# Performance work log

Hardware: AMD Instinct MI355X
Metric: run time of the kernel (lower is better)

Reference implementation:

```python
import jax, jax.numpy as jnp
import numpy as np

KERNEL = 7
PAD = 3


def setup_inputs() -> dict:
    key = jax.random.key(0)
    k1, k2, k3 = jax.random.split(key, 3)
    B, C, H, W = 16, 256, 64, 64
    x = jax.random.normal(k1, (B, C, H, W), dtype=jnp.float32)
    weight = jax.random.normal(k2, (C, KERNEL * KERNEL), dtype=jnp.float32)
    bias = jax.random.normal(k3, (C,), dtype=jnp.float32)
    return {"x": x, "weight": weight, "bias": bias}


def reference(x, weight, bias):
    # x: (B, C, H, W); weight: (C, K*K) laid out row-major as in nn.Unfold
    # (unfold * weight).sum over the K*K patch dim == depthwise 'same' conv.
    C = weight.shape[0]
    kernel = weight.reshape(C, 1, KERNEL, KERNEL)  # OIHW with I=1, groups=C
    out = jax.lax.conv_general_dilated(
        x, kernel,
        window_strides=(1, 1),
        padding=((PAD, PAD), (PAD, PAD)),
        dimension_numbers=("NCHW", "OIHW", "NCHW"),
        feature_group_count=C,
    )
    out = out + bias[None, :, None, None]
    # Original wraps this in to_sparse(): a lossless repacking of nonzero
    # pixels into (indices, features) with data-dependent shape. Its dense()
    # equals `out`, so we return the dense form.
    return out
```

## Files before the change

### kernel.cpp

```cpp
#include <hip/hip_runtime.h>


typedef _Float16 v2h __attribute__((ext_vector_type(2)));

static __device__ __forceinline__ v2h pack2(float a, float b) {
    return __builtin_bit_cast(v2h, __builtin_amdgcn_cvt_pkrtz(a, b));
}

__global__ __launch_bounds__(256, 2)
void dwconv7x7_dot2(const float* __restrict__ x,
                    const float* __restrict__ weight,
                    const float* __restrict__ bias,
                    float* __restrict__ out) {
    const int tid  = threadIdx.x;
    const int lane = tid & 63;
    const int wid  = tid >> 6;
    const int gw   = blockIdx.x * 4 + wid;
    const int plane = gw >> 1;
    const int half  = gw & 1;
    const int c = __builtin_amdgcn_readfirstlane(plane & 255);

    const float* wp = weight + c * 49;
    float wk[49];
#pragma unroll
    for (int k = 0; k < 49; ++k) wk[k] = wp[k];
    const float bv = bias[c];

    v2h  W[7][3];
    float w6[7];
#pragma unroll
    for (int kr = 0; kr < 7; ++kr) {
#pragma unroll
        for (int t = 0; t < 3; ++t) {
            v2h p = pack2(wk[kr * 7 + 2 * t], wk[kr * 7 + 2 * t + 1]);
            int b = __builtin_amdgcn_readfirstlane(__builtin_bit_cast(int, p));
            W[kr][t] = __builtin_bit_cast(v2h, b);
        }
        w6[kr] = wk[kr * 7 + 6];
    }

    const int tx = lane & 15;
    const int sy = lane >> 4;
    const int wb = tx * 4;
    const int hb = half * 32 + sy * 8;

    const float* xp = x + (size_t)plane * 4096;
    const int offm = (tx > 0)  ? (wb - 4) : wb;
    const int offp = (tx < 15) ? (wb + 4) : wb;

    float acc[8][4];
#pragma unroll
    for (int i = 0; i < 8; ++i)
#pragma unroll
        for (int j = 0; j < 4; ++j) acc[i][j] = 0.f;

#pragma unroll
    for (int j = 0; j < 14; ++j) {
        const int r  = hb - 3 + j;
        const int rc = min(max(r, 0), 63);
        const float* rowp = xp + rc * 64;
        const bool mrow = (r >= 0) && (r < 64);
        const bool mm = mrow && (tx > 0);
        const bool mp = mrow && (tx < 15);

        float4 qm = *reinterpret_cast<const float4*>(rowp + offm);
        float4 q0 = *reinterpret_cast<const float4*>(rowp + wb);
        float4 qp = *reinterpret_cast<const float4*>(rowp + offp);

        float f[10];
        f[0] = mm   ? qm.y : 0.f;
        f[1] = mm   ? qm.z : 0.f;
        f[2] = mm   ? qm.w : 0.f;
        f[3] = mrow ? q0.x : 0.f;
        f[4] = mrow ? q0.y : 0.f;
        f[5] = mrow ? q0.z : 0.f;
        f[6] = mrow ? q0.w : 0.f;
        f[7] = mp   ? qp.x : 0.f;
        f[8] = mp   ? qp.y : 0.f;
        f[9] = mp   ? qp.z : 0.f;

        v2h pk[8];
#pragma unroll
        for (int t = 0; t < 8; ++t) pk[t] = pack2(f[t], f[t + 1]);

#pragma unroll
        for (int oi = 0; oi < 8; ++oi) {
            const int kr = j - oi;
            if (kr >= 0 && kr < 7) {
#pragma unroll
                for (int jj = 0; jj < 4; ++jj) {
                    float a = fmaf(f[jj + 6], w6[kr], acc[oi][jj]);
                    a = __builtin_amdgcn_fdot2(pk[jj + 4], W[kr][2], a, false);
                    a = __builtin_amdgcn_fdot2(pk[jj + 2], W[kr][1], a, false);
                    a = __builtin_amdgcn_fdot2(pk[jj],     W[kr][0], a, false);
                    acc[oi][jj] = a;
                }
            }
        }
    }

    float* op = out + (size_t)plane * 4096 + (size_t)hb * 64 + wb;
#pragma unroll
    for (int oi = 0; oi < 8; ++oi) {
        float4 v;
        v.x = acc[oi][0] + bv;
        v.y = acc[oi][1] + bv;
        v.z = acc[oi][2] + bv;
        v.w = acc[oi][3] + bv;
        *reinterpret_cast<float4*>(op + oi * 64) = v;
    }
}

extern "C" void kernel_launch(void* const* d_in, const int* in_sizes, int n_in,
                              void* d_out, int out_size, void* d_ws, size_t ws_size,
                              hipStream_t stream) {
    const float* x      = (const float*)d_in[0];
    const float* weight = (const float*)d_in[1];
    const float* bias   = (const float*)d_in[2];
    float* out          = (float*)d_out;
    (void)in_sizes; (void)n_in; (void)out_size; (void)d_ws; (void)ws_size;

    dim3 grid(2048);
    dim3 block(256);
    dwconv7x7_dot2<<<grid, block, 0, stream>>>(x, weight, bias, out);
}
```

Measured before the change: 34.25 us.

## Roll row loop with sliding accumulator window and streaming output stores

Replaces the fully unrolled 14-row loop with a rolled loop that keeps a 7-row sliding window of accumulators, shifting them each iteration and storing one finished output row per step. This is meant to cut code size and register pressure. In exchange, it computes all 7 kernel-row updates for every input row, including boundary rows whose results are discarded, and it adds register-shift moves each iteration.

```diff
diff --git a/kernel.cpp b/kernel.cpp
--- a/kernel.cpp
+++ b/kernel.cpp
@@ -8,10 +8,10 @@
 }
 
 __global__ __launch_bounds__(256, 2)
-void dwconv7x7_dot2(const float* __restrict__ x,
-                    const float* __restrict__ weight,
-                    const float* __restrict__ bias,
-                    float* __restrict__ out) {
+void dwconv7x7_rolled(const float* __restrict__ x,
+                      const float* __restrict__ weight,
+                      const float* __restrict__ bias,
+                      float* __restrict__ out) {
     const int tid  = threadIdx.x;
     const int lane = tid & 63;
     const int wid  = tid >> 6;
@@ -48,13 +48,15 @@
     const int offm = (tx > 0)  ? (wb - 4) : wb;
     const int offp = (tx < 15) ? (wb + 4) : wb;
 
-    float acc[8][4];
+    float accR[7][4];
 #pragma unroll
-    for (int i = 0; i < 8; ++i)
+    for (int k = 0; k < 7; ++k)
 #pragma unroll
-        for (int j = 0; j < 4; ++j) acc[i][j] = 0.f;
+        for (int jj = 0; jj < 4; ++jj) accR[k][jj] = 0.f;
 
-#pragma unroll
+    float* op = out + (size_t)plane * 4096 + (size_t)hb * 64 + wb;
+
+#pragma unroll 1
     for (int j = 0; j < 14; ++j) {
         const int r  = hb - 3 + j;
         const int rc = min(max(r, 0), 63);
@@ -84,30 +86,33 @@
         for (int t = 0; t < 8; ++t) pk[t] = pack2(f[t], f[t + 1]);
 
 #pragma unroll
-        for (int oi = 0; oi < 8; ++oi) {
-            const int kr = j - oi;
-            if (kr >= 0 && kr < 7) {
+        for (int k = 0; k < 7; ++k) {
+            const int kr = 6 - k;
 #pragma unroll
-                for (int jj = 0; jj < 4; ++jj) {
-                    float a = fmaf(f[jj + 6], w6[kr], acc[oi][jj]);
-                    a = __builtin_amdgcn_fdot2(pk[jj + 4], W[kr][2], a, false);
-                    a = __builtin_amdgcn_fdot2(pk[jj + 2], W[kr][1], a, false);
-                    a = __builtin_amdgcn_fdot2(pk[jj],     W[kr][0], a, false);
-                    acc[oi][jj] = a;
-                }
+            for (int jj = 0; jj < 4; ++jj) {
+                float a = fmaf(f[jj + 6], w6[kr], accR[k][jj]);
+                a = __builtin_amdgcn_fdot2(pk[jj + 4], W[kr][2], a, false);
+                a = __builtin_amdgcn_fdot2(pk[jj + 2], W[kr][1], a, false);
+                a = __builtin_amdgcn_fdot2(pk[jj],     W[kr][0], a, false);
+                accR[k][jj] = a;
             }
         }
-    }
 
-    float* op = out + (size_t)plane * 4096 + (size_t)hb * 64 + wb;
+        if (j >= 6) {
+            float4 v;
+            v.x = accR[0][0] + bv;
+            v.y = accR[0][1] + bv;
+            v.z = accR[0][2] + bv;
+            v.w = accR[0][3] + bv;
+            *reinterpret_cast<float4*>(op + (j - 6) * 64) = v;
+        }
+
 #pragma unroll
-    for (int oi = 0; oi < 8; ++oi) {
-        float4 v;
-        v.x = acc[oi][0] + bv;
-        v.y = acc[oi][1] + bv;
-        v.z = acc[oi][2] + bv;
-        v.w = acc[oi][3] + bv;
-        *reinterpret_cast<float4*>(op + oi * 64) = v;
+        for (int k = 0; k < 6; ++k)
+#pragma unroll
+            for (int jj = 0; jj < 4; ++jj) accR[k][jj] = accR[k + 1][jj];
+#pragma unroll
+        for (int jj = 0; jj < 4; ++jj) accR[6][jj] = 0.f;
     }
 }
 
@@ -122,5 +127,5 @@
 
     dim3 grid(2048);
     dim3 block(256);
-    dwconv7x7_dot2<<<grid, block, 0, stream>>>(x, weight, bias, out);
+    dwconv7x7_rolled<<<grid, block, 0, stream>>>(x, weight, bias, out);
 }
```

After: 39.93 us. 16.6% more time.

## Flatten depthwise conv to one output row per thread with larger grid

Applied to the files above, without the earlier changes.

Replaces the register-blocked scheme, where each thread accumulated 8 output rows while streaming 14 input rows, with a flat scheme where each thread computes a single output row from 7 input rows. The grid grows eightfold so each block covers a quarter plane. This cuts register pressure and raises parallelism, but gives up vertical row reuse and quadruples redundant input loads per output, relying on caches. It also repeats the per-block weight loads many more times.

```diff
diff --git a/kernel.cpp b/kernel.cpp
--- a/kernel.cpp
+++ b/kernel.cpp
@@ -7,18 +7,15 @@
     return __builtin_bit_cast(v2h, __builtin_amdgcn_cvt_pkrtz(a, b));
 }
 
-__global__ __launch_bounds__(256, 2)
-void dwconv7x7_dot2(const float* __restrict__ x,
+__global__ __launch_bounds__(256)
+void dwconv7x7_flat(const float* __restrict__ x,
                     const float* __restrict__ weight,
                     const float* __restrict__ bias,
                     float* __restrict__ out) {
-    const int tid  = threadIdx.x;
-    const int lane = tid & 63;
-    const int wid  = tid >> 6;
-    const int gw   = blockIdx.x * 4 + wid;
-    const int plane = gw >> 1;
-    const int half  = gw & 1;
-    const int c = __builtin_amdgcn_readfirstlane(plane & 255);
+    const int tid   = threadIdx.x;
+    const int bk    = blockIdx.x;
+    const int plane = bk >> 2;
+    const int c     = plane & 255;
 
     const float* wp = weight + c * 49;
     float wk[49];
@@ -39,24 +36,20 @@
         w6[kr] = wk[kr * 7 + 6];
     }
 
-    const int tx = lane & 15;
-    const int sy = lane >> 4;
-    const int wb = tx * 4;
-    const int hb = half * 32 + sy * 8;
+    const int tx   = tid & 15;
+    const int ty   = tid >> 4;
+    const int orow = (bk & 3) * 16 + ty;
+    const int wb   = tx * 4;
 
     const float* xp = x + (size_t)plane * 4096;
     const int offm = (tx > 0)  ? (wb - 4) : wb;
     const int offp = (tx < 15) ? (wb + 4) : wb;
 
-    float acc[8][4];
-#pragma unroll
-    for (int i = 0; i < 8; ++i)
-#pragma unroll
-        for (int j = 0; j < 4; ++j) acc[i][j] = 0.f;
+    float a0 = 0.f, a1 = 0.f, a2 = 0.f, a3 = 0.f;
 
 #pragma unroll
-    for (int j = 0; j < 14; ++j) {
-        const int r  = hb - 3 + j;
+    for (int kr = 0; kr < 7; ++kr) {
+        const int r  = orow - 3 + kr;
         const int rc = min(max(r, 0), 63);
         const float* rowp = xp + rc * 64;
         const bool mrow = (r >= 0) && (r < 64);
@@ -83,32 +76,33 @@
 #pragma unroll
         for (int t = 0; t < 8; ++t) pk[t] = pack2(f[t], f[t + 1]);
 
-#pragma unroll
-        for (int oi = 0; oi < 8; ++oi) {
-            const int kr = j - oi;
-            if (kr >= 0 && kr < 7) {
-#pragma unroll
-                for (int jj = 0; jj < 4; ++jj) {
-                    float a = fmaf(f[jj + 6], w6[kr], acc[oi][jj]);
-                    a = __builtin_amdgcn_fdot2(pk[jj + 4], W[kr][2], a, false);
-                    a = __builtin_amdgcn_fdot2(pk[jj + 2], W[kr][1], a, false);
-                    a = __builtin_amdgcn_fdot2(pk[jj],     W[kr][0], a, false);
-                    acc[oi][jj] = a;
-                }
-            }
-        }
+        a0 = fmaf(f[6], w6[kr], a0);
+        a0 = __builtin_amdgcn_fdot2(pk[4], W[kr][2], a0, false);
+        a0 = __builtin_amdgcn_fdot2(pk[2], W[kr][1], a0, false);
+        a0 = __builtin_amdgcn_fdot2(pk[0], W[kr][0], a0, false);
+
+        a1 = fmaf(f[7], w6[kr], a1);
+        a1 = __builtin_amdgcn_fdot2(pk[5], W[kr][2], a1, false);
+        a1 = __builtin_amdgcn_fdot2(pk[3], W[kr][1], a1, false);
+        a1 = __builtin_amdgcn_fdot2(pk[1], W[kr][0], a1, false);
+
+        a2 = fmaf(f[8], w6[kr], a2);
+        a2 = __builtin_amdgcn_fdot2(pk[6], W[kr][2], a2, false);
+        a2 = __builtin_amdgcn_fdot2(pk[4], W[kr][1], a2, false);
+        a2 = __builtin_amdgcn_fdot2(pk[2], W[kr][0], a2, false);
+
+        a3 = fmaf(f[9], w6[kr], a3);
+        a3 = __builtin_amdgcn_fdot2(pk[7], W[kr][2], a3, false);
+        a3 = __builtin_amdgcn_fdot2(pk[5], W[kr][1], a3, false);
+        a3 = __builtin_amdgcn_fdot2(pk[3], W[kr][0], a3, false);
     }
 
-    float* op = out + (size_t)plane * 4096 + (size_t)hb * 64 + wb;
-#pragma unroll
-    for (int oi = 0; oi < 8; ++oi) {
-        float4 v;
-        v.x = acc[oi][0] + bv;
-        v.y = acc[oi][1] + bv;
-        v.z = acc[oi][2] + bv;
-        v.w = acc[oi][3] + bv;
-        *reinterpret_cast<float4*>(op + oi * 64) = v;
-    }
+    float4 v;
+    v.x = a0 + bv;
+    v.y = a1 + bv;
+    v.z = a2 + bv;
+    v.w = a3 + bv;
+    *reinterpret_cast<float4*>(out + (size_t)plane * 4096 + orow * 64 + wb) = v;
 }
 
 extern "C" void kernel_launch(void* const* d_in, const int* in_sizes, int n_in,
@@ -120,7 +114,7 @@
     float* out          = (float*)d_out;
     (void)in_sizes; (void)n_in; (void)out_size; (void)d_ws; (void)ws_size;
 
-    dim3 grid(2048);
+    dim3 grid(16384);
     dim3 block(256);
-    dwconv7x7_dot2<<<grid, block, 0, stream>>>(x, weight, bias, out);
+    dwconv7x7_flat<<<grid, block, 0, stream>>>(x, weight, bias, out);
 }
```

Result: slower. 48.29 us (+41.0%).
